# Kernel tuning notes

Measured on AMD Instinct MI355X. Metric: run time of the kernel, lower is better.

## Reference

```python
import jax, jax.numpy as jnp
import numpy as np

K = 16  # neighbors per node (knn_graph, loop=False)


def setup_inputs() -> dict:
    key = jax.random.key(0)
    ks = jax.random.split(key, 4)
    B, N = 32, 2048
    coords = jax.random.normal(ks[0], (B, N, 3), jnp.float32)

    def lin(k, i, o):  # glorot-ish init
        return jax.random.normal(k, (i, o), jnp.float32) / np.sqrt(i).astype(np.float32)

    return {
        "coords": coords,
        "W1": lin(ks[1], 3, 64),   "b1": jnp.zeros((64,), jnp.float32),
        "W2": lin(ks[2], 64, 128), "b2": jnp.zeros((128,), jnp.float32),
        "Wf": lin(ks[3], 128, 128), "bf": jnp.zeros((128,), jnp.float32),
    }


def _knn_idx(c, k):
    # c: [N,3] -> [N,k] indices of k nearest neighbors (self excluded, loop=False)
    n = c.shape[0]
    d2 = jnp.sum((c[:, None, :] - c[None, :, :]) ** 2, axis=-1)  # [N,N]
    d2 = jnp.where(jnp.eye(n, dtype=bool), jnp.inf, d2)
    _, idx = jax.lax.top_k(-d2, k)  # smallest distances
    return idx


def _gcn(x, nbr_self, W, b):
    # PyG GCNConv with add_self_loops: every node has in-degree exactly k+1
    # (k knn edges + self-loop), so the symmetric gcn_norm
    # 1/sqrt(deg_i*deg_j) reduces to the constant 1/(k+1).
    h = x @ W                                   # [N,out]
    agg = h[nbr_self].sum(axis=1) / nbr_self.shape[1]
    return agg + b


def reference(coords, W1, b1, W2, b2, Wf, bf):
    n = coords.shape[1]

    def per_sample(c):
        nbr = _knn_idx(c, K)                                     # [N,K]
        nbr_self = jnp.concatenate([nbr, jnp.arange(n)[:, None]], axis=1)  # [N,K+1]
        x = jax.nn.relu(_gcn(c, nbr_self, W1, b1))
        x = jax.nn.relu(_gcn(x, nbr_self, W2, b2))
        return x @ Wf + bf                                       # [N,128]

    return jax.vmap(per_sample)(coords)  # [B,N,128]
```

## Files before the change

### kernel.cpp

```cpp
#include <hip/hip_runtime.h>
#include <hip/hip_bf16.h>

typedef unsigned int u32;
typedef __attribute__((ext_vector_type(8))) short bf16x8;
typedef __attribute__((ext_vector_type(4))) float f32x4;

#define N_NODES 2048
#define INF __builtin_inff()

__device__ __forceinline__ float bflo(u32 u){ return __uint_as_float(u << 16); }
__device__ __forceinline__ float bfhi(u32 u){ return __uint_as_float(u & 0xFFFF0000u); }
__device__ __forceinline__ u32 packbf(float a, float b){
  u32 ua = __float_as_uint(a), ub = __float_as_uint(b);
  u32 ra = (ua + 0x7FFFu + ((ua >> 16) & 1u)) >> 16;
  u32 rb = (ub + 0x7FFFu + ((ub >> 16) & 1u)) >> 16;
  return ra | (rb << 16);
}

__device__ __forceinline__ void ins16(float (&ad)[16], float v) {
#pragma unroll
  for (int t = 15; t >= 1; --t)
    ad[t] = __builtin_amdgcn_fmed3f(v, ad[t-1], ad[t]);
  ad[0] = fminf(ad[0], v);
}

__device__ __forceinline__ float dist2(float cx, float cy, float cz,
                                       float jx, float jy, float jz) {
  float dx = cx - jx, dy = cy - jy, dz = cz - jz;
  return fmaf(dz, dz, fmaf(dy, dy, dx * dx));
}

__global__ __launch_bounds__(256) void k1_knn_l1(
    const float* __restrict__ coords, const float* __restrict__ W1,
    const float* __restrict__ b1, int* __restrict__ nbr, u32* __restrict__ x1)
{
  __shared__ float xs[N_NODES], ys[N_NODES], zs[N_NODES];
  __shared__ float w1s[192];
  __shared__ float b1s[64];
  __shared__ u32   nbuf[64][16];
  __shared__ u32   ncnt[64];
  const int tid   = threadIdx.x;
  const int s     = blockIdx.x >> 5;
  const int chunk = blockIdx.x & 31;
  const float* cs = coords + (size_t)s * (N_NODES * 3);
  for (int k = tid; k < N_NODES; k += 256) {
    xs[k] = cs[3*k]; ys[k] = cs[3*k+1]; zs[k] = cs[3*k+2];
  }
  if (tid < 192) w1s[tid] = W1[tid];
  if (tid < 64)  { b1s[tid] = b1[tid]; ncnt[tid] = 0; }
  __syncthreads();

  const int node = (chunk << 6) + (tid >> 2);
  const int sub  = tid & 3;
  const int ln   = tid >> 2;
  const float cx = xs[node], cy = ys[node], cz = zs[node];

  float ad[16];
#pragma unroll
  for (int q = 0; q < 16; ++q) ad[q] = INF;

  const float4* xs4 = (const float4*)xs;
  const float4* ys4 = (const float4*)ys;
  const float4* zs4 = (const float4*)zs;

  for (int it = 0; it < 128; ++it) {
    const int v4 = (it << 2) + sub;
    float4 xv = xs4[v4], yv = ys4[v4], zv = zs4[v4];
    const int base = v4 << 2;
    float d0 = (base + 0 == node) ? INF : dist2(cx, cy, cz, xv.x, yv.x, zv.x);
    float d1 = (base + 1 == node) ? INF : dist2(cx, cy, cz, xv.y, yv.y, zv.y);
    float d2 = (base + 2 == node) ? INF : dist2(cx, cy, cz, xv.z, yv.z, zv.z);
    float d3 = (base + 3 == node) ? INF : dist2(cx, cy, cz, xv.w, yv.w, zv.w);
    ins16(ad, d0); ins16(ad, d1); ins16(ad, d2); ins16(ad, d3);
  }

  float bd[16];
#pragma unroll
  for (int q = 0; q < 16; ++q) bd[q] = __shfl(ad[q], tid ^ 1);
#pragma unroll
  for (int q = 0; q < 16; ++q) ad[q] = fminf(ad[q], bd[15 - q]);
#define CED(I, J) { float lo_ = fminf(ad[I], ad[J]); ad[J] = fmaxf(ad[I], ad[J]); ad[I] = lo_; }
  CED(0,8) CED(1,9) CED(2,10) CED(3,11) CED(4,12) CED(5,13) CED(6,14) CED(7,15)
  CED(0,4) CED(1,5) CED(2,6)  CED(3,7)  CED(8,12) CED(9,13) CED(10,14) CED(11,15)
  CED(0,2) CED(1,3) CED(4,6)  CED(5,7)  CED(8,10) CED(9,11) CED(12,14) CED(13,15)
  CED(0,1) CED(2,3) CED(4,5)  CED(6,7)  CED(8,9)  CED(10,11) CED(12,13) CED(14,15)
#undef CED
#pragma unroll
  for (int q = 0; q < 16; ++q) bd[q] = __shfl(ad[q], tid ^ 2);
#pragma unroll
  for (int q = 0; q < 16; ++q) ad[q] = fminf(ad[q], bd[15 - q]);
  float tau = ad[0];
#pragma unroll
  for (int q = 1; q < 16; ++q) tau = fmaxf(tau, ad[q]);

  for (int it = 0; it < 128; ++it) {
    const int v4 = (it << 2) + sub;
    float4 xv = xs4[v4], yv = ys4[v4], zv = zs4[v4];
    const int base = v4 << 2;
    float d0 = (base + 0 == node) ? INF : dist2(cx, cy, cz, xv.x, yv.x, zv.x);
    float d1 = (base + 1 == node) ? INF : dist2(cx, cy, cz, xv.y, yv.y, zv.y);
    float d2 = (base + 2 == node) ? INF : dist2(cx, cy, cz, xv.z, yv.z, zv.z);
    float d3 = (base + 3 == node) ? INF : dist2(cx, cy, cz, xv.w, yv.w, zv.w);
    if (d0 <= tau) { u32 p = atomicAdd(&ncnt[ln], 1u); if (p < 16u) nbuf[ln][p] = (u32)(base + 0); }
    if (d1 <= tau) { u32 p = atomicAdd(&ncnt[ln], 1u); if (p < 16u) nbuf[ln][p] = (u32)(base + 1); }
    if (d2 <= tau) { u32 p = atomicAdd(&ncnt[ln], 1u); if (p < 16u) nbuf[ln][p] = (u32)(base + 2); }
    if (d3 <= tau) { u32 p = atomicAdd(&ncnt[ln], 1u); if (p < 16u) nbuf[ln][p] = (u32)(base + 3); }
  }
  __syncthreads();

  const size_t gnode = ((size_t)s << 11) + node;
  uint4 nb = *(const uint4*)&nbuf[ln][sub << 2];
  *(int4*)(nbr + gnode * 16 + (sub << 2)) =
      make_int4((int)nb.x, (int)nb.y, (int)nb.z, (int)nb.w);

  float sx, sy, sz;
  if (sub == 0) { sx = cx; sy = cy; sz = cz; } else { sx = 0.f; sy = 0.f; sz = 0.f; }
  sx += xs[nb.x] + xs[nb.y] + xs[nb.z] + xs[nb.w];
  sy += ys[nb.x] + ys[nb.y] + ys[nb.z] + ys[nb.w];
  sz += zs[nb.x] + zs[nb.y] + zs[nb.z] + zs[nb.w];
  sx += __shfl_xor(sx, 1); sx += __shfl_xor(sx, 2);
  sy += __shfl_xor(sy, 1); sy += __shfl_xor(sy, 2);
  sz += __shfl_xor(sz, 1); sz += __shfl_xor(sz, 2);
  const float inv = 1.0f / 17.0f;
  float mx = sx * inv, my = sy * inv, mz = sz * inv;

  u32 pk[8];
#pragma unroll
  for (int oo = 0; oo < 16; oo += 2) {
    const int o = (sub << 4) + oo;
    float v0 = fmaf(mz, w1s[128+o],   fmaf(my, w1s[64+o],   fmaf(mx, w1s[o],   b1s[o])));
    float v1 = fmaf(mz, w1s[128+o+1], fmaf(my, w1s[64+o+1], fmaf(mx, w1s[o+1], b1s[o+1])));
    pk[oo >> 1] = packbf(fmaxf(v0, 0.0f), fmaxf(v1, 0.0f));
  }
  uint4* xo = (uint4*)(x1 + gnode * 32 + (sub << 3));
  xo[0] = make_uint4(pk[0], pk[1], pk[2], pk[3]);
  xo[1] = make_uint4(pk[4], pk[5], pk[6], pk[7]);
}

__global__ __launch_bounds__(256) void k2_gcn2(
    const u32* __restrict__ x1, const int* __restrict__ nbr,
    const float* __restrict__ W2, const float* __restrict__ b2,
    u32* __restrict__ x2)
{
  __shared__ uint4 AldsV[1024];
  __shared__ uint4 BhiV[1024];
  __shared__ uint4 BloV[1024];
  char* Alds = (char*)AldsV; char* Bhi = (char*)BhiV; char* Blo = (char*)BloV;
  const int tid   = threadIdx.x;
  const int node0 = blockIdx.x << 7;

#pragma unroll
  for (int i = 0; i < 32; ++i) {
    int e = tid + (i << 8);
    int k = e >> 7, n = e & 127;
    float w = W2[e];
    u32 hb = packbf(w, 0.0f) & 0xFFFFu;
    float whi = __uint_as_float(hb << 16);
    u32 lb = packbf(w - whi, 0.0f) & 0xFFFFu;
    int byte = n * 128 + ((2 * k) ^ ((n & 7) << 4));
    *(unsigned short*)(Bhi + byte) = (unsigned short)hb;
    *(unsigned short*)(Blo + byte) = (unsigned short)lb;
  }

  {
    const int r = tid >> 1, half = tid & 1;
    const size_t gnode = (size_t)node0 + r;
    const u32* selfp = x1 + gnode * 32 + half * 16;
    const u32* x1s   = x1 + ((gnode >> 11) << 11) * 32;
    const int* nb    = nbr + gnode * 16;
    float a[32];
#pragma unroll
    for (int q = 0; q < 4; ++q) {
      uint4 v = *(const uint4*)(selfp + (q << 2));
      a[8*q+0] = bflo(v.x); a[8*q+1] = bfhi(v.x);
      a[8*q+2] = bflo(v.y); a[8*q+3] = bfhi(v.y);
      a[8*q+4] = bflo(v.z); a[8*q+5] = bfhi(v.z);
      a[8*q+6] = bflo(v.w); a[8*q+7] = bfhi(v.w);
    }
#pragma unroll
    for (int t = 0; t < 16; ++t) {
      const u32* rp = x1s + (size_t)nb[t] * 32 + half * 16;
#pragma unroll
      for (int q = 0; q < 4; ++q) {
        uint4 v = *(const uint4*)(rp + (q << 2));
        a[8*q+0] += bflo(v.x); a[8*q+1] += bfhi(v.x);
        a[8*q+2] += bflo(v.y); a[8*q+3] += bfhi(v.y);
        a[8*q+4] += bflo(v.z); a[8*q+5] += bfhi(v.z);
        a[8*q+6] += bflo(v.w); a[8*q+7] += bfhi(v.w);
      }
    }
    const float inv = 1.0f / 17.0f;
    u32 pk[16];
#pragma unroll
    for (int j = 0; j < 16; ++j)
      pk[j] = packbf(a[2*j] * inv, a[2*j+1] * inv);
#pragma unroll
    for (int q = 0; q < 4; ++q) {
      int byte = r * 128 + ((((half << 6) + (q << 4))) ^ ((r & 7) << 4));
      *(uint4*)(Alds + byte) = make_uint4(pk[4*q], pk[4*q+1], pk[4*q+2], pk[4*q+3]);
    }
  }
  __syncthreads();

  const int lane = tid & 63, wv = tid >> 6;
  const int cl = lane & 15, kg = lane >> 4;

  f32x4 acc[2][8];
#pragma unroll
  for (int rt = 0; rt < 2; ++rt)
#pragma unroll
    for (int ct = 0; ct < 8; ++ct) {
      float bv = b2[(ct << 4) + cl];
      acc[rt][ct] = (f32x4){bv, bv, bv, bv};
    }

#pragma unroll
  for (int ks = 0; ks < 2; ++ks) {
    const int kb = (ks << 6) + (kg << 4);
    bf16x8 af[2];
#pragma unroll
    for (int rt = 0; rt < 2; ++rt) {
      int row = (wv << 5) + (rt << 4) + cl;
      af[rt] = *(const bf16x8*)(Alds + row * 128 + (kb ^ ((row & 7) << 4)));
    }
#pragma unroll
    for (int ct = 0; ct < 8; ++ct) {
      int n = (ct << 4) + cl;
      int byte = n * 128 + (kb ^ ((n & 7) << 4));
      bf16x8 bh = *(const bf16x8*)(Bhi + byte);
      bf16x8 bl = *(const bf16x8*)(Blo + byte);
#pragma unroll
      for (int rt = 0; rt < 2; ++rt) {
        acc[rt][ct] = __builtin_amdgcn_mfma_f32_16x16x32_bf16(af[rt], bh, acc[rt][ct], 0, 0, 0);
        acc[rt][ct] = __builtin_amdgcn_mfma_f32_16x16x32_bf16(af[rt], bl, acc[rt][ct], 0, 0, 0);
      }
    }
  }

  unsigned short* x2h = (unsigned short*)x2;
#pragma unroll
  for (int rt = 0; rt < 2; ++rt)
#pragma unroll
    for (int ct = 0; ct < 8; ++ct) {
      int colg = (ct << 4) + cl;
      int nr0  = node0 + (wv << 5) + (rt << 4) + (kg << 2);
#pragma unroll
      for (int r = 0; r < 4; ++r) {
        float v = fmaxf(acc[rt][ct][r], 0.0f);
        x2h[(size_t)(nr0 + r) * 128 + colg] = (unsigned short)(packbf(v, 0.0f) & 0xFFFFu);
      }
    }
}

__global__ __launch_bounds__(256) void k3_final(
    const u32* __restrict__ x2, const float* __restrict__ Wf,
    const float* __restrict__ bfv, float* __restrict__ out)
{
  __shared__ uint4 AldsV[2048];
  __shared__ uint4 BhiV[1024];
  __shared__ uint4 BloV[1024];
  char* Alds = (char*)AldsV; char* Bhi = (char*)BhiV; char* Blo = (char*)BloV;
  const int tid   = threadIdx.x;
  const int node0 = (blockIdx.x >> 1) << 7;
  const int ch0   = (blockIdx.x & 1) << 6;

#pragma unroll
  for (int i = 0; i < 32; ++i) {
    int e = tid + (i << 8);
    int k = e >> 6, n = e & 63;
    float w = Wf[k * 128 + ch0 + n];
    u32 hb = packbf(w, 0.0f) & 0xFFFFu;
    float whi = __uint_as_float(hb << 16);
    u32 lb = packbf(w - whi, 0.0f) & 0xFFFFu;
    int byte = n * 256 + ((2 * k) ^ ((n & 15) << 4));
    *(unsigned short*)(Bhi + byte) = (unsigned short)hb;
    *(unsigned short*)(Blo + byte) = (unsigned short)lb;
  }

  {
    const int r = tid >> 1, half = tid & 1;
    const u32* src = x2 + (size_t)(node0 + r) * 64 + half * 32;
#pragma unroll
    for (int q = 0; q < 8; ++q) {
      uint4 v = *(const uint4*)(src + (q << 2));
      int byte = r * 256 + ((((half << 7) + (q << 4))) ^ ((r & 15) << 4));
      *(uint4*)(Alds + byte) = v;
    }
  }
  __syncthreads();

  const int lane = tid & 63, wv = tid >> 6;
  const int cl = lane & 15, kg = lane >> 4;

  f32x4 acc[2][4];
#pragma unroll
  for (int rt = 0; rt < 2; ++rt)
#pragma unroll
    for (int ct = 0; ct < 4; ++ct) {
      float bv = bfv[ch0 + (ct << 4) + cl];
      acc[rt][ct] = (f32x4){bv, bv, bv, bv};
    }

#pragma unroll
  for (int ks = 0; ks < 4; ++ks) {
    const int kb = (ks << 6) + (kg << 4);
    bf16x8 af[2];
#pragma unroll
    for (int rt = 0; rt < 2; ++rt) {
      int row = (wv << 5) + (rt << 4) + cl;
      af[rt] = *(const bf16x8*)(Alds + row * 256 + (kb ^ ((row & 15) << 4)));
    }
#pragma unroll
    for (int ct = 0; ct < 4; ++ct) {
      int n = (ct << 4) + cl;
      int byte = n * 256 + (kb ^ ((n & 15) << 4));
      bf16x8 bh = *(const bf16x8*)(Bhi + byte);
      bf16x8 bl = *(const bf16x8*)(Blo + byte);
#pragma unroll
      for (int rt = 0; rt < 2; ++rt) {
        acc[rt][ct] = __builtin_amdgcn_mfma_f32_16x16x32_bf16(af[rt], bh, acc[rt][ct], 0, 0, 0);
        acc[rt][ct] = __builtin_amdgcn_mfma_f32_16x16x32_bf16(af[rt], bl, acc[rt][ct], 0, 0, 0);
      }
    }
  }

#pragma unroll
  for (int rt = 0; rt < 2; ++rt)
#pragma unroll
    for (int ct = 0; ct < 4; ++ct) {
      int col = ch0 + (ct << 4) + cl;
      int nr0 = node0 + (wv << 5) + (rt << 4) + (kg << 2);
#pragma unroll
      for (int r = 0; r < 4; ++r)
        out[(size_t)(nr0 + r) * 128 + col] = acc[rt][ct][r];
    }
}

extern "C" void kernel_launch(void* const* d_in, const int* in_sizes, int n_in,
                              void* d_out, int out_size, void* d_ws, size_t ws_size,
                              hipStream_t stream) {
  const float* coords = (const float*)d_in[0];
  const float* W1 = (const float*)d_in[1];
  const float* b1 = (const float*)d_in[2];
  const float* W2 = (const float*)d_in[3];
  const float* b2 = (const float*)d_in[4];
  const float* Wf = (const float*)d_in[5];
  const float* bf = (const float*)d_in[6];
  float* out = (float*)d_out;

  char* ws = (char*)d_ws;
  int* nbr = (int*)ws;
  u32* x1  = (u32*)(ws + (size_t)4  * 1024 * 1024);
  u32* x2  = (u32*)(ws + (size_t)12 * 1024 * 1024);

  k1_knn_l1<<<1024, 256, 0, stream>>>(coords, W1, b1, nbr, x1);
  k2_gcn2  <<< 512, 256, 0, stream>>>(x1, nbr, W2, b2, x2);
  k3_final <<<1024, 256, 0, stream>>>(x2, Wf, bf, out);
}
```

Baseline: 189.6 us.

## Prefilter kNN candidates with a sampled threshold before exact top-16 selection

```diff
diff --git a/kernel.cpp b/kernel.cpp
--- a/kernel.cpp
+++ b/kernel.cpp
@@ -7,6 +7,7 @@
 
 #define N_NODES 2048
 #define INF __builtin_inff()
+#define SCAP 88
 
 __device__ __forceinline__ float bflo(u32 u){ return __uint_as_float(u << 16); }
 __device__ __forceinline__ float bfhi(u32 u){ return __uint_as_float(u & 0xFFFF0000u); }
@@ -30,15 +31,41 @@
   return fmaf(dz, dz, fmaf(dy, dy, dx * dx));
 }
 
+__device__ __forceinline__ void merge4(float (&ad)[16], int tid) {
+  float bd[16];
+#pragma unroll
+  for (int q = 0; q < 16; ++q) bd[q] = __shfl(ad[q], tid ^ 1);
+#pragma unroll
+  for (int q = 0; q < 16; ++q) ad[q] = fminf(ad[q], bd[15 - q]);
+#define CED(I, J) { float lo_ = fminf(ad[I], ad[J]); ad[J] = fmaxf(ad[I], ad[J]); ad[I] = lo_; }
+  CED(0,8) CED(1,9) CED(2,10) CED(3,11) CED(4,12) CED(5,13) CED(6,14) CED(7,15)
+  CED(0,4) CED(1,5) CED(2,6)  CED(3,7)  CED(8,12) CED(9,13) CED(10,14) CED(11,15)
+  CED(0,2) CED(1,3) CED(4,6)  CED(5,7)  CED(8,10) CED(9,11) CED(12,14) CED(13,15)
+  CED(0,1) CED(2,3) CED(4,5)  CED(6,7)  CED(8,9)  CED(10,11) CED(12,13) CED(14,15)
+#undef CED
+#pragma unroll
+  for (int q = 0; q < 16; ++q) bd[q] = __shfl(ad[q], tid ^ 2);
+#pragma unroll
+  for (int q = 0; q < 16; ++q) ad[q] = fminf(ad[q], bd[15 - q]);
+}
+
+__device__ __forceinline__ float max16(const float (&ad)[16]) {
+  float t = ad[0];
+#pragma unroll
+  for (int q = 1; q < 16; ++q) t = fmaxf(t, ad[q]);
+  return t;
+}
+
 __global__ __launch_bounds__(256) void k1_knn_l1(
     const float* __restrict__ coords, const float* __restrict__ W1,
     const float* __restrict__ b1, int* __restrict__ nbr, u32* __restrict__ x1)
 {
   __shared__ float xs[N_NODES], ys[N_NODES], zs[N_NODES];
+  __shared__ u32   sbuf[64][SCAP];
+  __shared__ u32   nbuf[64][16];
+  __shared__ u32   scnt[64], ncnt[64];
   __shared__ float w1s[192];
   __shared__ float b1s[64];
-  __shared__ u32   nbuf[64][16];
-  __shared__ u32   ncnt[64];
   const int tid   = threadIdx.x;
   const int s     = blockIdx.x >> 5;
   const int chunk = blockIdx.x & 31;
@@ -47,7 +74,7 @@
     xs[k] = cs[3*k]; ys[k] = cs[3*k+1]; zs[k] = cs[3*k+2];
   }
   if (tid < 192) w1s[tid] = W1[tid];
-  if (tid < 64)  { b1s[tid] = b1[tid]; ncnt[tid] = 0; }
+  if (tid < 64)  { b1s[tid] = b1[tid]; scnt[tid] = 0; ncnt[tid] = 0; }
   __syncthreads();
 
   const int node = (chunk << 6) + (tid >> 2);
@@ -55,15 +82,14 @@
   const int ln   = tid >> 2;
   const float cx = xs[node], cy = ys[node], cz = zs[node];
 
-  float ad[16];
-#pragma unroll
-  for (int q = 0; q < 16; ++q) ad[q] = INF;
-
   const float4* xs4 = (const float4*)xs;
   const float4* ys4 = (const float4*)ys;
   const float4* zs4 = (const float4*)zs;
 
-  for (int it = 0; it < 128; ++it) {
+  float ad[16];
+#pragma unroll
+  for (int q = 0; q < 16; ++q) ad[q] = INF;
+  for (int it = 0; it < 32; ++it) {
     const int v4 = (it << 2) + sub;
     float4 xv = xs4[v4], yv = ys4[v4], zv = zs4[v4];
     const int base = v4 << 2;
@@ -73,38 +99,76 @@
     float d3 = (base + 3 == node) ? INF : dist2(cx, cy, cz, xv.w, yv.w, zv.w);
     ins16(ad, d0); ins16(ad, d1); ins16(ad, d2); ins16(ad, d3);
   }
-
-  float bd[16];
-#pragma unroll
-  for (int q = 0; q < 16; ++q) bd[q] = __shfl(ad[q], tid ^ 1);
-#pragma unroll
-  for (int q = 0; q < 16; ++q) ad[q] = fminf(ad[q], bd[15 - q]);
-#define CED(I, J) { float lo_ = fminf(ad[I], ad[J]); ad[J] = fmaxf(ad[I], ad[J]); ad[I] = lo_; }
-  CED(0,8) CED(1,9) CED(2,10) CED(3,11) CED(4,12) CED(5,13) CED(6,14) CED(7,15)
-  CED(0,4) CED(1,5) CED(2,6)  CED(3,7)  CED(8,12) CED(9,13) CED(10,14) CED(11,15)
-  CED(0,2) CED(1,3) CED(4,6)  CED(5,7)  CED(8,10) CED(9,11) CED(12,14) CED(13,15)
-  CED(0,1) CED(2,3) CED(4,5)  CED(6,7)  CED(8,9)  CED(10,11) CED(12,13) CED(14,15)
-#undef CED
-#pragma unroll
-  for (int q = 0; q < 16; ++q) bd[q] = __shfl(ad[q], tid ^ 2);
-#pragma unroll
-  for (int q = 0; q < 16; ++q) ad[q] = fminf(ad[q], bd[15 - q]);
-  float tau = ad[0];
-#pragma unroll
-  for (int q = 1; q < 16; ++q) tau = fmaxf(tau, ad[q]);
+  merge4(ad, tid);
+  const float tauh = max16(ad);
 
   for (int it = 0; it < 128; ++it) {
     const int v4 = (it << 2) + sub;
     float4 xv = xs4[v4], yv = ys4[v4], zv = zs4[v4];
     const int base = v4 << 2;
-    float d0 = (base + 0 == node) ? INF : dist2(cx, cy, cz, xv.x, yv.x, zv.x);
-    float d1 = (base + 1 == node) ? INF : dist2(cx, cy, cz, xv.y, yv.y, zv.y);
-    float d2 = (base + 2 == node) ? INF : dist2(cx, cy, cz, xv.z, yv.z, zv.z);
-    float d3 = (base + 3 == node) ? INF : dist2(cx, cy, cz, xv.w, yv.w, zv.w);
-    if (d0 <= tau) { u32 p = atomicAdd(&ncnt[ln], 1u); if (p < 16u) nbuf[ln][p] = (u32)(base + 0); }
-    if (d1 <= tau) { u32 p = atomicAdd(&ncnt[ln], 1u); if (p < 16u) nbuf[ln][p] = (u32)(base + 1); }
-    if (d2 <= tau) { u32 p = atomicAdd(&ncnt[ln], 1u); if (p < 16u) nbuf[ln][p] = (u32)(base + 2); }
-    if (d3 <= tau) { u32 p = atomicAdd(&ncnt[ln], 1u); if (p < 16u) nbuf[ln][p] = (u32)(base + 3); }
+    float d0 = dist2(cx, cy, cz, xv.x, yv.x, zv.x);
+    float d1 = dist2(cx, cy, cz, xv.y, yv.y, zv.y);
+    float d2 = dist2(cx, cy, cz, xv.z, yv.z, zv.z);
+    float d3 = dist2(cx, cy, cz, xv.w, yv.w, zv.w);
+    if (d0 <= tauh && base + 0 != node) { u32 p = atomicAdd(&scnt[ln], 1u); if (p < SCAP) sbuf[ln][p] = (u32)(base + 0); }
+    if (d1 <= tauh && base + 1 != node) { u32 p = atomicAdd(&scnt[ln], 1u); if (p < SCAP) sbuf[ln][p] = (u32)(base + 1); }
+    if (d2 <= tauh && base + 2 != node) { u32 p = atomicAdd(&scnt[ln], 1u); if (p < SCAP) sbuf[ln][p] = (u32)(base + 2); }
+    if (d3 <= tauh && base + 3 != node) { u32 p = atomicAdd(&scnt[ln], 1u); if (p < SCAP) sbuf[ln][p] = (u32)(base + 3); }
+  }
+  __syncthreads();
+
+  const u32 cnt = scnt[ln];
+  const bool fb = (bool)__any((int)(cnt > SCAP));
+
+  if (!fb) {
+    float a2[16];
+#pragma unroll
+    for (int q = 0; q < 16; ++q) a2[q] = INF;
+#pragma unroll 2
+    for (int q = sub; q < SCAP; q += 4) {
+      u32 j = sbuf[ln][q] & (N_NODES - 1);
+      float d = dist2(cx, cy, cz, xs[j], ys[j], zs[j]);
+      ins16(a2, ((u32)q < cnt) ? d : INF);
+    }
+    merge4(a2, tid);
+    const float tau = max16(a2);
+#pragma unroll 2
+    for (int q = sub; q < SCAP; q += 4) {
+      u32 j = sbuf[ln][q] & (N_NODES - 1);
+      float d = dist2(cx, cy, cz, xs[j], ys[j], zs[j]);
+      if ((u32)q < cnt && d <= tau) {
+        u32 p = atomicAdd(&ncnt[ln], 1u); if (p < 16u) nbuf[ln][p] = j;
+      }
+    }
+  } else {
+    float a3[16];
+#pragma unroll
+    for (int q = 0; q < 16; ++q) a3[q] = INF;
+    for (int it = 0; it < 128; ++it) {
+      const int v4 = (it << 2) + sub;
+      float4 xv = xs4[v4], yv = ys4[v4], zv = zs4[v4];
+      const int base = v4 << 2;
+      float d0 = (base + 0 == node) ? INF : dist2(cx, cy, cz, xv.x, yv.x, zv.x);
+      float d1 = (base + 1 == node) ? INF : dist2(cx, cy, cz, xv.y, yv.y, zv.y);
+      float d2 = (base + 2 == node) ? INF : dist2(cx, cy, cz, xv.z, yv.z, zv.z);
+      float d3 = (base + 3 == node) ? INF : dist2(cx, cy, cz, xv.w, yv.w, zv.w);
+      ins16(a3, d0); ins16(a3, d1); ins16(a3, d2); ins16(a3, d3);
+    }
+    merge4(a3, tid);
+    const float tau = max16(a3);
+    for (int it = 0; it < 128; ++it) {
+      const int v4 = (it << 2) + sub;
+      float4 xv = xs4[v4], yv = ys4[v4], zv = zs4[v4];
+      const int base = v4 << 2;
+      float d0 = dist2(cx, cy, cz, xv.x, yv.x, zv.x);
+      float d1 = dist2(cx, cy, cz, xv.y, yv.y, zv.y);
+      float d2 = dist2(cx, cy, cz, xv.z, yv.z, zv.z);
+      float d3 = dist2(cx, cy, cz, xv.w, yv.w, zv.w);
+      if (d0 <= tau && base + 0 != node) { u32 p = atomicAdd(&ncnt[ln], 1u); if (p < 16u) nbuf[ln][p] = (u32)(base + 0); }
+      if (d1 <= tau && base + 1 != node) { u32 p = atomicAdd(&ncnt[ln], 1u); if (p < 16u) nbuf[ln][p] = (u32)(base + 1); }
+      if (d2 <= tau && base + 2 != node) { u32 p = atomicAdd(&ncnt[ln], 1u); if (p < 16u) nbuf[ln][p] = (u32)(base + 2); }
+      if (d3 <= tau && base + 3 != node) { u32 p = atomicAdd(&ncnt[ln], 1u); if (p < 16u) nbuf[ln][p] = (u32)(base + 3); }
+    }
   }
   __syncthreads();
 
```

Result: slower. 317.9 us (+67.7%).

## Pack neighbor index into distance key bits and keep top-12 per sub-lane

Applied to the files above, without the earlier changes.

```diff
diff --git a/kernel.cpp b/kernel.cpp
--- a/kernel.cpp
+++ b/kernel.cpp
@@ -17,17 +17,51 @@
   return ra | (rb << 16);
 }
 
-__device__ __forceinline__ void ins16(float (&ad)[16], float v) {
-#pragma unroll
-  for (int t = 15; t >= 1; --t)
-    ad[t] = __builtin_amdgcn_fmed3f(v, ad[t-1], ad[t]);
-  ad[0] = fminf(ad[0], v);
-}
-
 __device__ __forceinline__ float dist2(float cx, float cy, float cz,
                                        float jx, float jy, float jz) {
   float dx = cx - jx, dy = cy - jy, dz = cz - jz;
   return fmaf(dz, dz, fmaf(dy, dy, dx * dx));
+}
+
+__device__ __forceinline__ float mkkey(float d, int j, int node) {
+  u32 kb = (__float_as_uint(d) & 0xFFFFF800u) | (u32)j;
+  if (j == node) kb = 0x7E000000u;
+  return __uint_as_float(kb);
+}
+
+__device__ __forceinline__ void ins12(float (&ad)[12], float v) {
+#pragma unroll
+  for (int t = 11; t >= 1; --t)
+    ad[t] = __builtin_amdgcn_fmed3f(v, ad[t-1], ad[t]);
+  ad[0] = fminf(ad[0], v);
+}
+__device__ __forceinline__ void ins16(float (&ad)[16], float v) {
+#pragma unroll
+  for (int t = 15; t >= 1; --t)
+    ad[t] = __builtin_amdgcn_fmed3f(v, ad[t-1], ad[t]);
+  ad[0] = fminf(ad[0], v);
+}
+
+__device__ __forceinline__ void merge4s(float (&ad)[16], int tid) {
+#define CED(I, J) { float lo_ = fminf(ad[I], ad[J]); ad[J] = fmaxf(ad[I], ad[J]); ad[I] = lo_; }
+#define CLEAN16 \
+  CED(0,8) CED(1,9) CED(2,10) CED(3,11) CED(4,12) CED(5,13) CED(6,14) CED(7,15) \
+  CED(0,4) CED(1,5) CED(2,6)  CED(3,7)  CED(8,12) CED(9,13) CED(10,14) CED(11,15) \
+  CED(0,2) CED(1,3) CED(4,6)  CED(5,7)  CED(8,10) CED(9,11) CED(12,14) CED(13,15) \
+  CED(0,1) CED(2,3) CED(4,5)  CED(6,7)  CED(8,9)  CED(10,11) CED(12,13) CED(14,15)
+  float bd[16];
+#pragma unroll
+  for (int q = 0; q < 16; ++q) bd[q] = __shfl(ad[q], tid ^ 1);
+#pragma unroll
+  for (int q = 0; q < 16; ++q) ad[q] = fminf(ad[q], bd[15 - q]);
+  CLEAN16
+#pragma unroll
+  for (int q = 0; q < 16; ++q) bd[q] = __shfl(ad[q], tid ^ 2);
+#pragma unroll
+  for (int q = 0; q < 16; ++q) ad[q] = fminf(ad[q], bd[15 - q]);
+  CLEAN16
+#undef CLEAN16
+#undef CED
 }
 
 __global__ __launch_bounds__(256) void k1_knn_l1(
@@ -35,10 +69,10 @@
     const float* __restrict__ b1, int* __restrict__ nbr, u32* __restrict__ x1)
 {
   __shared__ float xs[N_NODES], ys[N_NODES], zs[N_NODES];
+  __shared__ u32   nbuf[64][16];
+  __shared__ u32   ncnt[64];
   __shared__ float w1s[192];
   __shared__ float b1s[64];
-  __shared__ u32   nbuf[64][16];
-  __shared__ u32   ncnt[64];
   const int tid   = threadIdx.x;
   const int s     = blockIdx.x >> 5;
   const int chunk = blockIdx.x & 31;
@@ -47,7 +81,7 @@
     xs[k] = cs[3*k]; ys[k] = cs[3*k+1]; zs[k] = cs[3*k+2];
   }
   if (tid < 192) w1s[tid] = W1[tid];
-  if (tid < 64)  { b1s[tid] = b1[tid]; ncnt[tid] = 0; }
+  if (tid < 64)  b1s[tid] = b1[tid];
   __syncthreads();
 
   const int node = (chunk << 6) + (tid >> 2);
@@ -55,69 +89,99 @@
   const int ln   = tid >> 2;
   const float cx = xs[node], cy = ys[node], cz = zs[node];
 
-  float ad[16];
-#pragma unroll
-  for (int q = 0; q < 16; ++q) ad[q] = INF;
-
   const float4* xs4 = (const float4*)xs;
   const float4* ys4 = (const float4*)ys;
   const float4* zs4 = (const float4*)zs;
 
-  for (int it = 0; it < 128; ++it) {
-    const int v4 = (it << 2) + sub;
-    float4 xv = xs4[v4], yv = ys4[v4], zv = zs4[v4];
-    const int base = v4 << 2;
-    float d0 = (base + 0 == node) ? INF : dist2(cx, cy, cz, xv.x, yv.x, zv.x);
-    float d1 = (base + 1 == node) ? INF : dist2(cx, cy, cz, xv.y, yv.y, zv.y);
-    float d2 = (base + 2 == node) ? INF : dist2(cx, cy, cz, xv.z, yv.z, zv.z);
-    float d3 = (base + 3 == node) ? INF : dist2(cx, cy, cz, xv.w, yv.w, zv.w);
-    ins16(ad, d0); ins16(ad, d1); ins16(ad, d2); ins16(ad, d3);
-  }
-
-  float bd[16];
-#pragma unroll
-  for (int q = 0; q < 16; ++q) bd[q] = __shfl(ad[q], tid ^ 1);
-#pragma unroll
-  for (int q = 0; q < 16; ++q) ad[q] = fminf(ad[q], bd[15 - q]);
-#define CED(I, J) { float lo_ = fminf(ad[I], ad[J]); ad[J] = fmaxf(ad[I], ad[J]); ad[I] = lo_; }
-  CED(0,8) CED(1,9) CED(2,10) CED(3,11) CED(4,12) CED(5,13) CED(6,14) CED(7,15)
-  CED(0,4) CED(1,5) CED(2,6)  CED(3,7)  CED(8,12) CED(9,13) CED(10,14) CED(11,15)
-  CED(0,2) CED(1,3) CED(4,6)  CED(5,7)  CED(8,10) CED(9,11) CED(12,14) CED(13,15)
-  CED(0,1) CED(2,3) CED(4,5)  CED(6,7)  CED(8,9)  CED(10,11) CED(12,13) CED(14,15)
-#undef CED
-#pragma unroll
-  for (int q = 0; q < 16; ++q) bd[q] = __shfl(ad[q], tid ^ 2);
-#pragma unroll
-  for (int q = 0; q < 16; ++q) ad[q] = fminf(ad[q], bd[15 - q]);
-  float tau = ad[0];
-#pragma unroll
-  for (int q = 1; q < 16; ++q) tau = fmaxf(tau, ad[q]);
-
-  for (int it = 0; it < 128; ++it) {
-    const int v4 = (it << 2) + sub;
-    float4 xv = xs4[v4], yv = ys4[v4], zv = zs4[v4];
-    const int base = v4 << 2;
-    float d0 = (base + 0 == node) ? INF : dist2(cx, cy, cz, xv.x, yv.x, zv.x);
-    float d1 = (base + 1 == node) ? INF : dist2(cx, cy, cz, xv.y, yv.y, zv.y);
-    float d2 = (base + 2 == node) ? INF : dist2(cx, cy, cz, xv.z, yv.z, zv.z);
-    float d3 = (base + 3 == node) ? INF : dist2(cx, cy, cz, xv.w, yv.w, zv.w);
-    if (d0 <= tau) { u32 p = atomicAdd(&ncnt[ln], 1u); if (p < 16u) nbuf[ln][p] = (u32)(base + 0); }
-    if (d1 <= tau) { u32 p = atomicAdd(&ncnt[ln], 1u); if (p < 16u) nbuf[ln][p] = (u32)(base + 1); }
-    if (d2 <= tau) { u32 p = atomicAdd(&ncnt[ln], 1u); if (p < 16u) nbuf[ln][p] = (u32)(base + 2); }
-    if (d3 <= tau) { u32 p = atomicAdd(&ncnt[ln], 1u); if (p < 16u) nbuf[ln][p] = (u32)(base + 3); }
-  }
-  __syncthreads();
+  float ad[12];
+#pragma unroll
+  for (int q = 0; q < 12; ++q) ad[q] = INF;
+
+  for (int it = 0; it < 64; ++it) {
+    const int v4a = (it << 3) + sub, v4b = v4a + 4;
+    float4 xa = xs4[v4a], ya = ys4[v4a], za = zs4[v4a];
+    float4 xb = xs4[v4b], yb = ys4[v4b], zb = zs4[v4b];
+    const int ba = v4a << 2, bb = v4b << 2;
+    ins12(ad, mkkey(dist2(cx,cy,cz, xa.x,ya.x,za.x), ba+0, node));
+    ins12(ad, mkkey(dist2(cx,cy,cz, xa.y,ya.y,za.y), ba+1, node));
+    ins12(ad, mkkey(dist2(cx,cy,cz, xa.z,ya.z,za.z), ba+2, node));
+    ins12(ad, mkkey(dist2(cx,cy,cz, xa.w,ya.w,za.w), ba+3, node));
+    ins12(ad, mkkey(dist2(cx,cy,cz, xb.x,yb.x,zb.x), bb+0, node));
+    ins12(ad, mkkey(dist2(cx,cy,cz, xb.y,yb.y,zb.y), bb+1, node));
+    ins12(ad, mkkey(dist2(cx,cy,cz, xb.z,yb.z,zb.z), bb+2, node));
+    ins12(ad, mkkey(dist2(cx,cy,cz, xb.w,yb.w,zb.w), bb+3, node));
+  }
+
+  const float myMax = ad[11];
+  float md[16];
+#pragma unroll
+  for (int q = 0; q < 12; ++q) md[q] = ad[q];
+  md[12] = md[13] = md[14] = md[15] = __uint_as_float(0x7F000000u);
+  merge4s(md, tid);
+
+  const float md15 = md[15];
+  float mnext = INF;
+#pragma unroll
+  for (int q = 11; q >= 0; --q) mnext = (ad[q] > md15) ? ad[q] : mnext;
+  float cand17 = fminf(mnext, __shfl(mnext, tid ^ 1));
+  cand17 = fminf(cand17, __shfl(cand17, tid ^ 2));
+
+  const u32 t15 = __float_as_uint(md15)   & 0xFFFFF800u;
+  const u32 t17 = __float_as_uint(cand17) & 0xFFFFF800u;
+  const bool ok = (myMax >= cand17) & (t17 >= t15 + 0x800u);
+
+  int j0, j1, j2, j3;
+  if (__all((int)ok)) {
+    j0 = (int)(__float_as_uint(md[(sub<<2)+0]) & 0x7FFu);
+    j1 = (int)(__float_as_uint(md[(sub<<2)+1]) & 0x7FFu);
+    j2 = (int)(__float_as_uint(md[(sub<<2)+2]) & 0x7FFu);
+    j3 = (int)(__float_as_uint(md[(sub<<2)+3]) & 0x7FFu);
+  } else {
+    float a3[16];
+#pragma unroll
+    for (int q = 0; q < 16; ++q) a3[q] = INF;
+#pragma unroll 1
+    for (int it = 0; it < 128; ++it) {
+      const int v4 = (it << 2) + sub;
+      float4 xv = xs4[v4], yv = ys4[v4], zv = zs4[v4];
+      const int base = v4 << 2;
+      float d0 = (base + 0 == node) ? INF : dist2(cx,cy,cz, xv.x,yv.x,zv.x);
+      float d1 = (base + 1 == node) ? INF : dist2(cx,cy,cz, xv.y,yv.y,zv.y);
+      float d2 = (base + 2 == node) ? INF : dist2(cx,cy,cz, xv.z,yv.z,zv.z);
+      float d3 = (base + 3 == node) ? INF : dist2(cx,cy,cz, xv.w,yv.w,zv.w);
+      ins16(a3, d0); ins16(a3, d1); ins16(a3, d2); ins16(a3, d3);
+    }
+    merge4s(a3, tid);
+    const float tau = a3[15];
+    if (sub == 0) ncnt[ln] = 0;
+    asm volatile("s_waitcnt lgkmcnt(0)" ::: "memory");
+#pragma unroll 1
+    for (int it = 0; it < 128; ++it) {
+      const int v4 = (it << 2) + sub;
+      float4 xv = xs4[v4], yv = ys4[v4], zv = zs4[v4];
+      const int base = v4 << 2;
+      float d0 = dist2(cx,cy,cz, xv.x,yv.x,zv.x);
+      float d1 = dist2(cx,cy,cz, xv.y,yv.y,zv.y);
+      float d2 = dist2(cx,cy,cz, xv.z,yv.z,zv.z);
+      float d3 = dist2(cx,cy,cz, xv.w,yv.w,zv.w);
+      if (d0 <= tau && base + 0 != node) { u32 p = atomicAdd(&ncnt[ln], 1u); if (p < 16u) nbuf[ln][p] = (u32)(base + 0); }
+      if (d1 <= tau && base + 1 != node) { u32 p = atomicAdd(&ncnt[ln], 1u); if (p < 16u) nbuf[ln][p] = (u32)(base + 1); }
+      if (d2 <= tau && base + 2 != node) { u32 p = atomicAdd(&ncnt[ln], 1u); if (p < 16u) nbuf[ln][p] = (u32)(base + 2); }
+      if (d3 <= tau && base + 3 != node) { u32 p = atomicAdd(&ncnt[ln], 1u); if (p < 16u) nbuf[ln][p] = (u32)(base + 3); }
+    }
+    asm volatile("s_waitcnt lgkmcnt(0)" ::: "memory");
+    uint4 nb4 = *(const uint4*)&nbuf[ln][sub << 2];
+    j0 = (int)nb4.x; j1 = (int)nb4.y; j2 = (int)nb4.z; j3 = (int)nb4.w;
+  }
 
   const size_t gnode = ((size_t)s << 11) + node;
-  uint4 nb = *(const uint4*)&nbuf[ln][sub << 2];
-  *(int4*)(nbr + gnode * 16 + (sub << 2)) =
-      make_int4((int)nb.x, (int)nb.y, (int)nb.z, (int)nb.w);
+  *(int4*)(nbr + gnode * 16 + (sub << 2)) = make_int4(j0, j1, j2, j3);
 
   float sx, sy, sz;
   if (sub == 0) { sx = cx; sy = cy; sz = cz; } else { sx = 0.f; sy = 0.f; sz = 0.f; }
-  sx += xs[nb.x] + xs[nb.y] + xs[nb.z] + xs[nb.w];
-  sy += ys[nb.x] + ys[nb.y] + ys[nb.z] + ys[nb.w];
-  sz += zs[nb.x] + zs[nb.y] + zs[nb.z] + zs[nb.w];
+  sx += xs[j0] + xs[j1] + xs[j2] + xs[j3];
+  sy += ys[j0] + ys[j1] + ys[j2] + ys[j3];
+  sz += zs[j0] + zs[j1] + zs[j2] + zs[j3];
   sx += __shfl_xor(sx, 1); sx += __shfl_xor(sx, 2);
   sy += __shfl_xor(sy, 1); sy += __shfl_xor(sy, 2);
   sz += __shfl_xor(sz, 1); sz += __shfl_xor(sz, 2);
```

After: 208.6 us. 10.0% more time.
